# Optimization experiments

Hardware: AMD Instinct MI355X
Metric: run time of the kernel (lower is better)

The kernel has to match this reference:

```python
import jax, jax.numpy as jnp
import numpy as np

THRESHOLD = 1.0
DECAY = 0.9
SURR_SLOPE = 10.0

B, T, IN, HID, OUT = 1024, 16, 2312, 1024, 10


def setup_inputs() -> dict:
    key = jax.random.key(0)
    kx, kw1, kb1, kw2, kb2 = jax.random.split(key, 5)
    x = jax.random.normal(kx, (B, T, IN), dtype=jnp.float32)
    # PyTorch nn.Linear default init: U(-1/sqrt(fan_in), 1/sqrt(fan_in))
    lim1 = 1.0 / np.sqrt(IN)
    lim2 = 1.0 / np.sqrt(HID)
    W1 = jax.random.uniform(kw1, (HID, IN), jnp.float32, -lim1, lim1)
    b1 = jax.random.uniform(kb1, (HID,), jnp.float32, -lim1, lim1)
    W2 = jax.random.uniform(kw2, (OUT, HID), jnp.float32, -lim2, lim2)
    b2 = jax.random.uniform(kb2, (OUT,), jnp.float32, -lim2, lim2)
    return {"x": x, "W1": W1, "b1": b1, "W2": W2, "b2": b2}


def _lif_step(v, inp):
    # leaky integrate-and-fire with sigmoid surrogate spike
    v_new = DECAY * v + inp
    spike = jax.nn.sigmoid(SURR_SLOPE * (v_new - THRESHOLD))
    v_next = v_new * (1.0 - spike)
    return v_next, spike


def reference(x, W1, b1, W2, b2):
    # x: [B, T, IN] -> spikes: [B, T, OUT]
    Bn = x.shape[0]
    v1_0 = jnp.zeros((Bn, W1.shape[0]), x.dtype)
    v2_0 = jnp.zeros((Bn, W2.shape[0]), x.dtype)

    # Precompute the first linear over all time steps (batched GEMM).
    h_all = jnp.einsum('bti,hi->bth', x, W1) + b1  # [B, T, HID]

    def step(carry, h_t):
        v1, v2 = carry
        v1, s1 = _lif_step(v1, h_t)                 # [B, HID]
        o_t = s1 @ W2.T + b2                        # [B, OUT]
        v2, s2 = _lif_step(v2, o_t)
        return (v1, v2), s2

    h_tb = jnp.swapaxes(h_all, 0, 1)                # [T, B, HID]
    _, spikes = jax.lax.scan(step, (v1_0, v2_0), h_tb)
    return jnp.swapaxes(spikes, 0, 1)               # [B, T, OUT]
```

## Files before the change

kernel.cpp:

```cpp
#include <hip/hip_runtime.h>

typedef _Float16 half8  __attribute__((ext_vector_type(8)));
typedef _Float16 half4v __attribute__((ext_vector_type(4)));
typedef float    floatx4 __attribute__((ext_vector_type(4)));

#define K_DIM 2312
#define KP    2368
#define N_DIM 1024
#define M_DIM 16384
#define T_DIM 16
#define O_DIM 10
#define NKT   74
#define NT_OLD 73
#define LDP 40

__global__ __launch_bounds__(256) void cvt_f32_f16_pad(const float* __restrict__ src,
                                                       _Float16* __restrict__ dst) {
  int row = blockIdx.x;
  const float* s = src + (size_t)row * K_DIM;
  _Float16* d = dst + (size_t)row * KP;
  for (int c = threadIdx.x; c < 296; c += 256) {
    half8 o;
    if (c < 289) {
      floatx4 a = *(const floatx4*)(s + c * 8);
      floatx4 b = *(const floatx4*)(s + c * 8 + 4);
      #pragma unroll
      for (int e = 0; e < 4; ++e) { o[e] = (_Float16)a[e]; o[4 + e] = (_Float16)b[e]; }
    } else {
      o = half8{0, 0, 0, 0, 0, 0, 0, 0};
    }
    *(half8*)(d + c * 8) = o;
  }
}

__device__ __forceinline__ void gload16(const _Float16* g, _Float16* l) {
  __builtin_amdgcn_global_load_lds((const __attribute__((address_space(1))) void*)g,
                                   (__attribute__((address_space(3))) void*)l, 16, 0, 0);
}

__global__ __launch_bounds__(512, 2) void gemm_f16_256(const _Float16* __restrict__ A,
                                                       const _Float16* __restrict__ Bw,
                                                       const float* __restrict__ b1,
                                                       float* __restrict__ h) {
  __shared__ __align__(16) _Float16 As[4][256 * 32];
  __shared__ __align__(16) _Float16 Bs[4][256 * 32];

  const int tid  = threadIdx.x;
  const int lane = tid & 63;
  const int w    = tid >> 6;
  const int wm   = (w >> 2) * 128;
  const int wn   = (w & 3) * 64;
  const int bm   = blockIdx.x & 63;
  const int bn   = blockIdx.x >> 6;
  const int m0   = bm * 256;
  const int n0   = bn * 256;

  const int rlo = lane >> 2;
  const int key = (rlo >> 1) & 3;
  const int cch = (lane & 3) ^ key;
  const _Float16* ag = A  + (size_t)(m0 + w * 32 + rlo) * KP + cch * 8;
  const _Float16* bg = Bw + (size_t)(n0 + w * 32 + rlo) * KP + cch * 8;
  const int stb = (w * 32) * 32;

  floatx4 acc[8][4];
  #pragma unroll
  for (int i = 0; i < 8; ++i)
    #pragma unroll
    for (int j = 0; j < 4; ++j)
      acc[i][j] = floatx4{0.f, 0.f, 0.f, 0.f};

  const int fr  = lane & 15;
  const int g   = lane >> 4;
  const int rds = (g ^ ((fr >> 1) & 3)) * 8;
  int offA[8], offB[4];
  #pragma unroll
  for (int i = 0; i < 8; ++i) offA[i] = (wm + i * 16 + fr) * 32 + rds;
  #pragma unroll
  for (int j = 0; j < 4; ++j) offB[j] = (wn + j * 16 + fr) * 32 + rds;

  half8 af[8], bf[4];

#define STAGE(tk) do {                                                    \
    const int _s = (tk) & 3;                                              \
    gload16(ag + (tk) * 32,           &As[_s][stb]);                      \
    gload16(ag + (tk) * 32 + 16 * KP, &As[_s][stb + 16 * 32]);            \
    gload16(bg + (tk) * 32,           &Bs[_s][stb]);                      \
    gload16(bg + (tk) * 32 + 16 * KP, &Bs[_s][stb + 16 * 32]);            \
  } while (0)

#define READF(tk) do {                                                    \
    const int _s = (tk) & 3;                                              \
    _Pragma("unroll")                                                     \
    for (int _i = 0; _i < 8; ++_i) af[_i] = *(const half8*)(&As[_s][offA[_i]]); \
    _Pragma("unroll")                                                     \
    for (int _j = 0; _j < 4; ++_j) bf[_j] = *(const half8*)(&Bs[_s][offB[_j]]); \
  } while (0)

#define MFMA32 do {                                                       \
    __builtin_amdgcn_s_setprio(1);                                        \
    _Pragma("unroll")                                                     \
    for (int _i = 0; _i < 8; ++_i)                                        \
      _Pragma("unroll")                                                   \
      for (int _j = 0; _j < 4; ++_j)                                      \
        acc[_i][_j] = __builtin_amdgcn_mfma_f32_16x16x32_f16(af[_i], bf[_j], acc[_i][_j], 0, 0, 0); \
    __builtin_amdgcn_s_setprio(0);                                        \
  } while (0)

  STAGE(0); STAGE(1); STAGE(2);
  asm volatile("s_waitcnt vmcnt(8)" ::: "memory");
  __builtin_amdgcn_sched_barrier(0);
  __builtin_amdgcn_s_barrier();
  __builtin_amdgcn_sched_barrier(0);
  READF(0);

  for (int t = 0; t < NKT - 3; ++t) {
    STAGE(t + 3);
    asm volatile("s_waitcnt vmcnt(8)" ::: "memory");
    __builtin_amdgcn_sched_barrier(0);
    __builtin_amdgcn_s_barrier();
    __builtin_amdgcn_sched_barrier(0);
    MFMA32;
    READF(t + 1);
  }
  asm volatile("s_waitcnt vmcnt(4)" ::: "memory");
  __builtin_amdgcn_sched_barrier(0);
  __builtin_amdgcn_s_barrier();
  __builtin_amdgcn_sched_barrier(0);
  MFMA32;
  READF(NKT - 2);
  asm volatile("s_waitcnt vmcnt(0)" ::: "memory");
  __builtin_amdgcn_sched_barrier(0);
  __builtin_amdgcn_s_barrier();
  __builtin_amdgcn_sched_barrier(0);
  MFMA32;
  READF(NKT - 1);
  __builtin_amdgcn_s_barrier();
  __builtin_amdgcn_sched_barrier(0);
  MFMA32;

#undef STAGE
#undef READF
#undef MFMA32

  const int cr = (lane >> 4) * 4;
  #pragma unroll
  for (int j = 0; j < 4; ++j) {
    int col = n0 + wn + j * 16 + fr;
    float bv = b1[col];
    #pragma unroll
    for (int i = 0; i < 8; ++i) {
      int rbase = m0 + wm + i * 16 + cr;
      #pragma unroll
      for (int e = 0; e < 4; ++e)
        h[(size_t)(rbase + e) * N_DIM + col] = acc[i][j][e] + bv;
    }
  }
}

__device__ __forceinline__ void stage_load(const float* __restrict__ x,
                                           const float* __restrict__ w,
                                           int m0, int n0, int k0, int tid,
                                           floatx4 (&ar)[4], floatx4 (&br)[4]) {
  int r = tid >> 3;
  int c = (tid & 7) * 4;
  bool ok = (k0 + c) < K_DIM;
  #pragma unroll
  for (int i = 0; i < 4; ++i) {
    int row = r + 32 * i;
    if (ok) {
      ar[i] = *(const floatx4*)(x + (size_t)(m0 + row) * K_DIM + k0 + c);
      br[i] = *(const floatx4*)(w + (size_t)(n0 + row) * K_DIM + k0 + c);
    } else {
      ar[i] = floatx4{0.f, 0.f, 0.f, 0.f};
      br[i] = floatx4{0.f, 0.f, 0.f, 0.f};
    }
  }
}

__device__ __forceinline__ void stage_write(_Float16* __restrict__ Ab,
                                            _Float16* __restrict__ Bb, int tid,
                                            const floatx4 (&ar)[4], const floatx4 (&br)[4]) {
  int r = tid >> 3;
  int c = (tid & 7) * 4;
  #pragma unroll
  for (int i = 0; i < 4; ++i) {
    int row = r + 32 * i;
    half4v av, bv;
    #pragma unroll
    for (int e = 0; e < 4; ++e) {
      av[e] = (_Float16)ar[i][e];
      bv[e] = (_Float16)br[i][e];
    }
    *(half4v*)(Ab + row * LDP + c) = av;
    *(half4v*)(Bb + row * LDP + c) = bv;
  }
}

__global__ __launch_bounds__(256) void gemm1_kernel(const float* __restrict__ x,
                                                    const float* __restrict__ W1,
                                                    const float* __restrict__ b1,
                                                    float* __restrict__ h) {
  __shared__ _Float16 Al[2][128 * LDP];
  __shared__ _Float16 Bl[2][128 * LDP];

  int tid  = threadIdx.x;
  int lane = tid & 63;
  int w    = tid >> 6;
  int wm   = (w >> 1) * 64;
  int wn   = (w & 1) * 64;
  int m0   = (blockIdx.x >> 3) * 128;
  int n0   = (blockIdx.x & 7) * 128;

  floatx4 acc[4][4];
  #pragma unroll
  for (int i = 0; i < 4; ++i)
    #pragma unroll
    for (int j = 0; j < 4; ++j)
      acc[i][j] = floatx4{0.f, 0.f, 0.f, 0.f};

  floatx4 ar[4], br[4];
  stage_load(x, W1, m0, n0, 0, tid, ar, br);
  stage_write(Al[0], Bl[0], tid, ar, br);
  __syncthreads();

  int fr = lane & 15;
  int kc = (lane >> 4) * 8;

  int cur = 0;
  for (int kt = 0; kt < NT_OLD; ++kt) {
    if (kt + 1 < NT_OLD) stage_load(x, W1, m0, n0, (kt + 1) * 32, tid, ar, br);

    const _Float16* Ab = Al[cur];
    const _Float16* Bb = Bl[cur];
    half8 af[4], bf[4];
    #pragma unroll
    for (int f = 0; f < 4; ++f) {
      af[f] = *(const half8*)(Ab + (wm + f * 16 + fr) * LDP + kc);
      bf[f] = *(const half8*)(Bb + (wn + f * 16 + fr) * LDP + kc);
    }
    #pragma unroll
    for (int i = 0; i < 4; ++i)
      #pragma unroll
      for (int j = 0; j < 4; ++j)
        acc[i][j] = __builtin_amdgcn_mfma_f32_16x16x32_f16(af[i], bf[j], acc[i][j], 0, 0, 0);

    if (kt + 1 < NT_OLD) stage_write(Al[cur ^ 1], Bl[cur ^ 1], tid, ar, br);
    __syncthreads();
    cur ^= 1;
  }

  int cr = (lane >> 4) * 4;
  #pragma unroll
  for (int j = 0; j < 4; ++j) {
    int col = n0 + wn + j * 16 + fr;
    float bv = b1[col];
    #pragma unroll
    for (int i = 0; i < 4; ++i) {
      int rbase = m0 + wm + i * 16 + cr;
      #pragma unroll
      for (int e = 0; e < 4; ++e)
        h[(size_t)(rbase + e) * N_DIM + col] = acc[i][j][e] + bv;
    }
  }
}

__global__ __launch_bounds__(256) void snn_temporal_kernel(const float* __restrict__ h,
                                                           const float* __restrict__ W2,
                                                           const float* __restrict__ b2,
                                                           float* __restrict__ out) {
  __shared__ float w2s[O_DIM * N_DIM];
  int tid = threadIdx.x;
  for (int i = tid; i < O_DIM * N_DIM; i += 256) w2s[i] = W2[i];
  __syncthreads();

  int wave = tid >> 6;
  int lane = tid & 63;
  int b = blockIdx.x * 4 + wave;
  const float* hrow = h + (size_t)b * (T_DIM * N_DIM);
  float* orow = out + (size_t)b * (T_DIM * O_DIM);

  float v1[16];
  #pragma unroll
  for (int e = 0; e < 16; ++e) v1[e] = 0.f;
  float v2 = 0.f;
  float bias2 = (lane < O_DIM) ? b2[lane] : 0.f;

  floatx4 hv[4];
  #pragma unroll
  for (int c = 0; c < 4; ++c) hv[c] = *(const floatx4*)(hrow + c * 256 + lane * 4);

  for (int t = 0; t < T_DIM; ++t) {
    floatx4 hn[4];
    if (t + 1 < T_DIM) {
      #pragma unroll
      for (int c = 0; c < 4; ++c)
        hn[c] = *(const floatx4*)(hrow + (t + 1) * N_DIM + c * 256 + lane * 4);
    }

    float sarr[16];
    #pragma unroll
    for (int c = 0; c < 4; ++c) {
      #pragma unroll
      for (int e = 0; e < 4; ++e) {
        int ii = c * 4 + e;
        float vn = 0.9f * v1[ii] + hv[c][e];
        float s  = 1.f / (1.f + __expf(10.f - 10.f * vn));
        v1[ii] = vn * (1.f - s);
        sarr[ii] = s;
      }
    }

    float part[10];
    #pragma unroll
    for (int o = 0; o < O_DIM; ++o) {
      float a = 0.f;
      #pragma unroll
      for (int c = 0; c < 4; ++c) {
        floatx4 w4 = *(const floatx4*)&w2s[o * N_DIM + c * 256 + lane * 4];
        a += sarr[c * 4 + 0] * w4[0] + sarr[c * 4 + 1] * w4[1]
           + sarr[c * 4 + 2] * w4[2] + sarr[c * 4 + 3] * w4[3];
      }
      part[o] = a;
    }
    #pragma unroll
    for (int m = 1; m < 64; m <<= 1) {
      #pragma unroll
      for (int o = 0; o < O_DIM; ++o) part[o] += __shfl_xor(part[o], m, 64);
    }

    float po = part[0];
    #pragma unroll
    for (int o = 1; o < O_DIM; ++o) po = (lane == o) ? part[o] : po;

    if (lane < O_DIM) {
      float vo = 0.9f * v2 + po + bias2;
      float s2 = 1.f / (1.f + __expf(10.f - 10.f * vo));
      v2 = vo * (1.f - s2);
      orow[t * O_DIM + lane] = s2;
    }

    #pragma unroll
    for (int c = 0; c < 4; ++c) hv[c] = hn[c];
  }
}

extern "C" void kernel_launch(void* const* d_in, const int* in_sizes, int n_in,
                              void* d_out, int out_size, void* d_ws, size_t ws_size,
                              hipStream_t stream) {
  const float* x  = (const float*)d_in[0];
  const float* W1 = (const float*)d_in[1];
  const float* b1 = (const float*)d_in[2];
  const float* W2 = (const float*)d_in[3];
  const float* b2 = (const float*)d_in[4];
  float* out = (float*)d_out;

  float* h = (float*)d_ws;

  const size_t H_BYTES  = (size_t)M_DIM * N_DIM * 4;
  const size_t XH_BYTES = (size_t)M_DIM * KP * 2;
  const size_t WH_BYTES = (size_t)N_DIM * KP * 2;
  const size_t NEED = H_BYTES + XH_BYTES + WH_BYTES;

  if (ws_size >= NEED) {
    _Float16* xh  = (_Float16*)((char*)d_ws + H_BYTES);
    _Float16* w1h = (_Float16*)((char*)d_ws + H_BYTES + XH_BYTES);
    cvt_f32_f16_pad<<<dim3(M_DIM), dim3(256), 0, stream>>>(x, xh);
    cvt_f32_f16_pad<<<dim3(N_DIM), dim3(256), 0, stream>>>(W1, w1h);
    gemm_f16_256<<<dim3(256), dim3(512), 0, stream>>>(xh, w1h, b1, h);
  } else {
    gemm1_kernel<<<dim3(1024), dim3(256), 0, stream>>>(x, W1, b1, h);
  }
  snn_temporal_kernel<<<dim3(256), dim3(256), 0, stream>>>(h, W2, b2, out);
}
```

Measured before the change: 154.3 us.

## Fuse fp32-to-fp16 conversion of x into the GEMM's A-tile loading

Removes the separate pass that converts x to padded fp16. The GEMM now loads fp32 x rows directly into registers, converts them, and writes swizzled fp16 into LDS. W1 is still staged with global_load_lds. The K loop drops to 73 tiles, and the tail tile is masked to zero past K=2312. This saves a full read and write of the 16384x2368 fp16 intermediate, at the cost of register-staged A loads, twice the global read bytes for A across the 4 N-blocks, and shallower LDS buffering (2 A stages, 3 B stages).

```diff
diff --git a/kernel.cpp b/kernel.cpp
--- a/kernel.cpp
+++ b/kernel.cpp
@@ -10,7 +10,7 @@
 #define M_DIM 16384
 #define T_DIM 16
 #define O_DIM 10
-#define NKT   74
+#define NKT   73
 #define NT_OLD 73
 #define LDP 40
 
@@ -38,12 +38,29 @@
                                    (__attribute__((address_space(3))) void*)l, 16, 0, 0);
 }
 
-__global__ __launch_bounds__(512, 2) void gemm_f16_256(const _Float16* __restrict__ A,
-                                                       const _Float16* __restrict__ Bw,
-                                                       const float* __restrict__ b1,
-                                                       float* __restrict__ h) {
-  __shared__ __align__(16) _Float16 As[4][256 * 32];
-  __shared__ __align__(16) _Float16 Bs[4][256 * 32];
+__device__ __forceinline__ half8 cvt8(floatx4 a, floatx4 b) {
+  half8 r;
+  #pragma unroll
+  for (int e = 0; e < 4; ++e) { r[e] = (_Float16)a[e]; r[4 + e] = (_Float16)b[e]; }
+  return r;
+}
+
+__device__ __forceinline__ half8 cvt8_masked(floatx4 a, floatx4 b, int kbase) {
+  half8 r;
+  #pragma unroll
+  for (int e = 0; e < 4; ++e) {
+    r[e]     = (kbase + e     < K_DIM) ? (_Float16)a[e] : (_Float16)0.f;
+    r[4 + e] = (kbase + 4 + e < K_DIM) ? (_Float16)b[e] : (_Float16)0.f;
+  }
+  return r;
+}
+
+__global__ __launch_bounds__(512, 2) void gemm_fused(const float* __restrict__ X,
+                                                     const _Float16* __restrict__ Bw,
+                                                     const float* __restrict__ b1,
+                                                     float* __restrict__ h) {
+  __shared__ __align__(16) _Float16 As[2][256 * 32];
+  __shared__ __align__(16) _Float16 Bs[3][256 * 32];
 
   const int tid  = threadIdx.x;
   const int lane = tid & 63;
@@ -55,12 +72,19 @@
   const int m0   = bm * 256;
   const int n0   = bn * 256;
 
-  const int rlo = lane >> 2;
-  const int key = (rlo >> 1) & 3;
-  const int cch = (lane & 3) ^ key;
-  const _Float16* ag = A  + (size_t)(m0 + w * 32 + rlo) * KP + cch * 8;
+  const int rA   = tid >> 1;
+  const int kA   = (tid & 1) * 16;
+  const int keyA = (rA >> 1) & 3;
+  const int gA   = kA >> 3;
+  const float* xa = X + (size_t)(m0 + rA) * K_DIM;
+  const int dstA0 = rA * 32 + ((gA    ) ^ keyA) * 8;
+  const int dstA1 = rA * 32 + ((gA + 1) ^ keyA) * 8;
+
+  const int rlo  = lane >> 2;
+  const int keyB = (rlo >> 1) & 3;
+  const int cch  = (lane & 3) ^ keyB;
   const _Float16* bg = Bw + (size_t)(n0 + w * 32 + rlo) * KP + cch * 8;
-  const int stb = (w * 32) * 32;
+  const int stbB = (w * 32) * 32;
 
   floatx4 acc[8][4];
   #pragma unroll
@@ -79,66 +103,100 @@
   for (int j = 0; j < 4; ++j) offB[j] = (wn + j * 16 + fr) * 32 + rds;
 
   half8 af[8], bf[4];
-
-#define STAGE(tk) do {                                                    \
-    const int _s = (tk) & 3;                                              \
-    gload16(ag + (tk) * 32,           &As[_s][stb]);                      \
-    gload16(ag + (tk) * 32 + 16 * KP, &As[_s][stb + 16 * 32]);            \
-    gload16(bg + (tk) * 32,           &Bs[_s][stb]);                      \
-    gload16(bg + (tk) * 32 + 16 * KP, &Bs[_s][stb + 16 * 32]);            \
+  floatx4 L0, L1, M0v, M1v;
+
+#define CLAMPK(k) ((k) > (K_DIM - 4) ? (K_DIM - 4) : (k))
+#define LOADL(ts) do { int _k = (ts) * 32 + kA;                              \
+    L0  = *(const floatx4*)(xa + CLAMPK(_k));                                \
+    L1  = *(const floatx4*)(xa + CLAMPK(_k + 4)); } while (0)
+#define LOADM(ts) do { int _k = (ts) * 32 + kA + 8;                          \
+    M0v = *(const floatx4*)(xa + CLAMPK(_k));                                \
+    M1v = *(const floatx4*)(xa + CLAMPK(_k + 4)); } while (0)
+#define STAGEB(ts) do { const int _s = (ts) % 3;                             \
+    gload16(bg + (ts) * 32,           &Bs[_s][stbB]);                        \
+    gload16(bg + (ts) * 32 + 16 * KP, &Bs[_s][stbB + 16 * 32]); } while (0)
+
+#define READF(tk) do {                                                       \
+    const _Float16* _A = As[(tk) & 1];                                       \
+    const _Float16* _B = Bs[(tk) % 3];                                       \
+    _Pragma("unroll")                                                        \
+    for (int _i = 0; _i < 8; ++_i) af[_i] = *(const half8*)(&_A[offA[_i]]);  \
+    _Pragma("unroll")                                                        \
+    for (int _j = 0; _j < 4; ++_j) bf[_j] = *(const half8*)(&_B[offB[_j]]);  \
   } while (0)
 
-#define READF(tk) do {                                                    \
-    const int _s = (tk) & 3;                                              \
-    _Pragma("unroll")                                                     \
-    for (int _i = 0; _i < 8; ++_i) af[_i] = *(const half8*)(&As[_s][offA[_i]]); \
-    _Pragma("unroll")                                                     \
-    for (int _j = 0; _j < 4; ++_j) bf[_j] = *(const half8*)(&Bs[_s][offB[_j]]); \
+#define MFMA32 do {                                                          \
+    __builtin_amdgcn_s_setprio(1);                                           \
+    _Pragma("unroll")                                                        \
+    for (int _i = 0; _i < 8; ++_i)                                           \
+      _Pragma("unroll")                                                      \
+      for (int _j = 0; _j < 4; ++_j)                                         \
+        acc[_i][_j] = __builtin_amdgcn_mfma_f32_16x16x32_f16(af[_i], bf[_j], acc[_i][_j], 0, 0, 0); \
+    __builtin_amdgcn_s_setprio(0);                                           \
   } while (0)
 
-#define MFMA32 do {                                                       \
-    __builtin_amdgcn_s_setprio(1);                                        \
-    _Pragma("unroll")                                                     \
-    for (int _i = 0; _i < 8; ++_i)                                        \
-      _Pragma("unroll")                                                   \
-      for (int _j = 0; _j < 4; ++_j)                                      \
-        acc[_i][_j] = __builtin_amdgcn_mfma_f32_16x16x32_f16(af[_i], bf[_j], acc[_i][_j], 0, 0, 0); \
-    __builtin_amdgcn_s_setprio(0);                                        \
-  } while (0)
-
-  STAGE(0); STAGE(1); STAGE(2);
-  asm volatile("s_waitcnt vmcnt(8)" ::: "memory");
+  LOADL(0); LOADM(0);
+  asm volatile("s_waitcnt vmcnt(0)" ::: "memory");
+  __builtin_amdgcn_sched_barrier(0);
+  *(half8*)(&As[0][dstA0]) = cvt8(L0, L1);
+  *(half8*)(&As[0][dstA1]) = cvt8(M0v, M1v);
+  STAGEB(0);
+  LOADL(1); LOADM(1);
+  STAGEB(1);
+  asm volatile("s_waitcnt vmcnt(0)" ::: "memory");
+  __builtin_amdgcn_sched_barrier(0);
+  asm volatile("s_waitcnt lgkmcnt(0)" ::: "memory");
   __builtin_amdgcn_sched_barrier(0);
   __builtin_amdgcn_s_barrier();
   __builtin_amdgcn_sched_barrier(0);
   READF(0);
 
-  for (int t = 0; t < NKT - 3; ++t) {
-    STAGE(t + 3);
-    asm volatile("s_waitcnt vmcnt(8)" ::: "memory");
+  for (int t = 0; t < NKT - 2; ++t) {
+    const int wsl = (t + 1) & 1;
+    asm volatile("s_waitcnt vmcnt(4)" ::: "memory");
+    __builtin_amdgcn_sched_barrier(0);
+    *(half8*)(&As[wsl][dstA0]) = cvt8(L0, L1);
+    LOADL(t + 2);
+    __builtin_amdgcn_sched_barrier(0);
+    asm volatile("s_waitcnt vmcnt(4)" ::: "memory");
+    __builtin_amdgcn_sched_barrier(0);
+    *(half8*)(&As[wsl][dstA1]) = cvt8(M0v, M1v);
+    LOADM(t + 2);
+    STAGEB(t + 2);
+    __builtin_amdgcn_sched_barrier(0);
+    asm volatile("s_waitcnt vmcnt(6)" ::: "memory");
+    __builtin_amdgcn_sched_barrier(0);
+    asm volatile("s_waitcnt lgkmcnt(0)" ::: "memory");
     __builtin_amdgcn_sched_barrier(0);
     __builtin_amdgcn_s_barrier();
     __builtin_amdgcn_sched_barrier(0);
     MFMA32;
     READF(t + 1);
   }
-  asm volatile("s_waitcnt vmcnt(4)" ::: "memory");
-  __builtin_amdgcn_sched_barrier(0);
-  __builtin_amdgcn_s_barrier();
-  __builtin_amdgcn_sched_barrier(0);
+
+  {
+    const int kb = (NKT - 1) * 32 + kA;
+    asm volatile("s_waitcnt vmcnt(4)" ::: "memory");
+    __builtin_amdgcn_sched_barrier(0);
+    *(half8*)(&As[(NKT - 1) & 1][dstA0]) = cvt8_masked(L0, L1, kb);
+    asm volatile("s_waitcnt vmcnt(2)" ::: "memory");
+    __builtin_amdgcn_sched_barrier(0);
+    *(half8*)(&As[(NKT - 1) & 1][dstA1]) = cvt8_masked(M0v, M1v, kb + 8);
+    asm volatile("s_waitcnt vmcnt(0)" ::: "memory");
+    __builtin_amdgcn_sched_barrier(0);
+    asm volatile("s_waitcnt lgkmcnt(0)" ::: "memory");
+    __builtin_amdgcn_sched_barrier(0);
+    __builtin_amdgcn_s_barrier();
+    __builtin_amdgcn_sched_barrier(0);
+    MFMA32;
+    READF(NKT - 1);
+  }
   MFMA32;
-  READF(NKT - 2);
-  asm volatile("s_waitcnt vmcnt(0)" ::: "memory");
-  __builtin_amdgcn_sched_barrier(0);
-  __builtin_amdgcn_s_barrier();
-  __builtin_amdgcn_sched_barrier(0);
-  MFMA32;
-  READF(NKT - 1);
-  __builtin_amdgcn_s_barrier();
-  __builtin_amdgcn_sched_barrier(0);
-  MFMA32;
-
-#undef STAGE
+
+#undef CLAMPK
+#undef LOADL
+#undef LOADM
+#undef STAGEB
 #undef READF
 #undef MFMA32
 
@@ -357,16 +415,13 @@
   float* h = (float*)d_ws;
 
   const size_t H_BYTES  = (size_t)M_DIM * N_DIM * 4;
-  const size_t XH_BYTES = (size_t)M_DIM * KP * 2;
   const size_t WH_BYTES = (size_t)N_DIM * KP * 2;
-  const size_t NEED = H_BYTES + XH_BYTES + WH_BYTES;
+  const size_t NEED = H_BYTES + WH_BYTES;
 
   if (ws_size >= NEED) {
-    _Float16* xh  = (_Float16*)((char*)d_ws + H_BYTES);
-    _Float16* w1h = (_Float16*)((char*)d_ws + H_BYTES + XH_BYTES);
-    cvt_f32_f16_pad<<<dim3(M_DIM), dim3(256), 0, stream>>>(x, xh);
+    _Float16* w1h = (_Float16*)((char*)d_ws + H_BYTES);
     cvt_f32_f16_pad<<<dim3(N_DIM), dim3(256), 0, stream>>>(W1, w1h);
-    gemm_f16_256<<<dim3(256), dim3(512), 0, stream>>>(xh, w1h, b1, h);
+    gemm_fused<<<dim3(256), dim3(512), 0, stream>>>(x, w1h, b1, h);
   } else {
     gemm1_kernel<<<dim3(1024), dim3(256), 0, stream>>>(x, W1, b1, h);
   }
```

Measured after the change: 143.5 us. -7.0%, faster.
